# Kernel optimization log

Measured on AMD Instinct MI355X. Metric: run time of the kernel, lower is better.

The kernel has to match this reference:

```python
import jax, jax.numpy as jnp
import numpy as np

B, D = 8, 256
MEM, CW, R, K, KL = 131072, 64, 4, 4, 4
C = R * K + 2 * KL + 1  # 25 visible cells
DELTA = 0.005
EPS = 1e-6
TIMESTEP = 1.0  # first step after reset


def _gather(x, idx):
    # x: (b,m) or (b,m,w); idx: (b,k)
    if x.ndim == 2:
        return jnp.take_along_axis(x, idx, axis=1)
    e = jnp.broadcast_to(idx[:, :, None], idx.shape + (x.shape[-1],))
    return jnp.take_along_axis(x, e, axis=1)


def _fwd(xi, memory, visible_memory, link_matrix, rev_link_matrix, precedence,
         read_weights, write_weights, usage,
         W_rq, b_rq, W_wv, b_wv, W_ig, b_ig, W_wg, b_wg,
         read_positions):
    b = xi.shape[0]
    bidx = jnp.arange(b)[:, None]

    # interface transforms (independent linears)
    read_query = (xi @ W_rq + b_rq).reshape(b, R, CW)      # (b,r,w)
    write_vector = (xi @ W_wv + b_wv).reshape(b, 1, CW)    # (b,1,w)
    ig = jax.nn.sigmoid(xi @ W_ig + b_ig)                  # (b,c)
    wg = jax.nn.sigmoid(xi @ W_wg + b_wg)                  # (b,1)

    # ------------------ write ------------------
    rw_vis = _gather(read_weights, read_positions)         # (b,c)
    ww_vis = _gather(write_weights, read_positions)        # (b,c)

    # usage update + least-used indicator over visible cells
    u = (rw_vis + ww_vis > DELTA).astype(memory.dtype)
    rel = _gather(usage, read_positions)
    I_min = (rel == jnp.min(rel, axis=-1, keepdims=True)).astype(memory.dtype)
    rel_new = (TIMESTEP - rel) * u + rel * (1.0 - u)
    usage = usage.at[bidx, read_positions].set(rel_new)

    # interpolated write weights over visible cells
    ww_new = wg * (ig * rw_vis + (1.0 - ig) * I_min)       # (b,c)
    write_weights = write_weights.at[bidx, read_positions].set(ww_new)

    # erase + write into visible memory, scatter back into sparse memory
    visible_memory = visible_memory * (1.0 - I_min[:, :, None]) + ww_new[:, :, None] * write_vector
    memory = memory.at[bidx, read_positions].set(visible_memory)

    # link matrix / reverse link matrix update
    trp = read_positions[:, R * K:R * K + 2 * KL]          # temporal positions (b,2KL)
    Ieye = jnp.eye(MEM, 2 * KL, dtype=memory.dtype)[None]  # eye(m,k) mask as in torch code
    prec_dense = jnp.zeros_like(write_weights).at[bidx, trp].set(precedence)  # (b,m)
    tww = _gather(write_weights, trp)                      # (b,2KL)
    link_matrix = ((1.0 - write_weights[:, :, None]) * link_matrix
                   + write_weights[:, :, None] * precedence[:, None, :]) * Ieye
    rev_link_matrix = ((1.0 - tww[:, None, :]) * rev_link_matrix
                       + tww[:, None, :] * prec_dense[:, :, None]) * Ieye

    # precedence update and least-used cell (argmin usage)
    precedence = (1.0 - jnp.sum(tww, axis=-1, keepdims=True)) * precedence + tww
    least_used = jax.lax.top_k(-usage, 1)[1]               # (b,1)

    # ------------------ read ------------------
    trw = _gather(read_weights, trp)                       # (b,2KL)
    fwd_w = jnp.einsum('bmk,bk->bm', link_matrix, trw)     # forward weighting
    bwd_w = jnp.einsum('bmk,bk->bm', rev_link_matrix, trw) # backward weighting

    # exact L2 k-NN over full memory (dense surrogate for the FAISS search)
    mem_sq = jnp.sum(memory * memory, axis=-1)             # (b,m)
    dots = jnp.einsum('brw,bmw->brm', read_query, memory)  # (b,r,m)
    knn = jax.lax.top_k(2.0 * dots - mem_sq[:, None, :], K)[1].reshape(b, R * K)

    fp = jax.lax.top_k(fwd_w, KL)[1]
    bp = jax.lax.top_k(bwd_w, KL)[1]
    lum = jnp.full((b, 1), C + 1, dtype=knn.dtype)         # timestep <= mem_size branch
    max_length = least_used[0, 0]                          # mem_limit_reached == False
    positions = jnp.clip(
        jnp.concatenate([knn, fp.astype(knn.dtype), bp.astype(knn.dtype), lum], axis=1),
        0, max_length)                                     # (b,c)

    visible = _gather(memory, positions)                   # (b,c,w)
    kq = read_query / (jnp.linalg.norm(read_query, axis=-1, keepdims=True) + EPS)
    vn = visible / (jnp.linalg.norm(visible, axis=-1, keepdims=True) + EPS)
    sim = jnp.einsum('brw,bcw->brc', kq, vn)               # cosine similarity
    rw_c = jax.nn.softmax(sim, axis=-1)                    # (b,r,c)
    read_vectors = jnp.einsum('brc,bcw->brw', rw_c, visible)
    return read_vectors


def setup_inputs() -> dict:
    key = jax.random.key(0)
    ks = jax.random.split(key, 16)
    inp = {}
    inp['xi'] = jax.random.normal(ks[0], (B, D), jnp.float32)
    inp['memory'] = jax.random.normal(ks[1], (B, MEM, CW), jnp.float32)
    inp['visible_memory'] = jax.random.normal(ks[2], (B, C, CW), jnp.float32)
    inp['link_matrix'] = 0.1 * jax.random.uniform(ks[3], (B, MEM, 2 * KL), jnp.float32)
    inp['rev_link_matrix'] = 0.1 * jax.random.uniform(ks[4], (B, MEM, 2 * KL), jnp.float32)
    inp['precedence'] = 0.1 * jax.random.uniform(ks[5], (B, 2 * KL), jnp.float32)
    inp['read_weights'] = 0.01 * jax.random.uniform(ks[6], (B, MEM), jnp.float32)
    inp['write_weights'] = 0.01 * jax.random.uniform(ks[7], (B, MEM), jnp.float32)
    usage = 0.5 + 0.5 * jax.random.uniform(ks[8], (B, MEM), jnp.float32)
    inp['usage'] = usage.at[:, MEM - 1].set(0.0)  # argmin lands at m-1 so the clamp is a no-op
    inp['least_used_mem'] = jnp.full((B, 1), MEM // 2, jnp.int32)
    inp['read_positions'] = jax.random.randint(ks[9], (B, C), 0, MEM)

    def lin(k, fi, fo):
        s = (6.0 / fi) ** 0.5  # kaiming-uniform-like
        return jax.random.uniform(k, (fi, fo), jnp.float32, -s, s)
    inp['W_rq'] = lin(ks[10], D, R * CW); inp['b_rq'] = jnp.zeros((R * CW,), jnp.float32)
    inp['W_wv'] = lin(ks[11], D, CW);     inp['b_wv'] = jnp.zeros((CW,), jnp.float32)
    inp['W_ig'] = lin(ks[12], D, C);      inp['b_ig'] = jnp.zeros((C,), jnp.float32)
    inp['W_wg'] = lin(ks[13], D, 1);      inp['b_wg'] = jnp.zeros((1,), jnp.float32)
    return inp


def reference(xi, memory, visible_memory, link_matrix, rev_link_matrix, precedence,
              read_weights, write_weights, usage, least_used_mem, read_positions,
              W_rq, b_rq, W_wv, b_wv, W_ig, b_ig, W_wg, b_wg):
    # least_used_mem is overwritten inside write() (argmin of updated usage) before use
    return _fwd(xi, memory, visible_memory, link_matrix, rev_link_matrix, precedence,
                read_weights, write_weights, usage,
                W_rq, b_rq, W_wv, b_wv, W_ig, b_ig, W_wg, b_wg,
                read_positions)
```

## Files before the change

### kernel.cpp

```cpp
#include <hip/hip_runtime.h>
#include <math.h>

#define BN 8
#define DDIM 256
#define MEMN 131072
#define CWN 64
#define RN 4
#define CN 25
#define DELTA_C 0.005f
#define EPS_C 1e-6f
#define RPB 1024
#define NBLK (MEMN / RPB)
#define NEG_INF (-3.402823466e38f)
#define IMAX 0x7fffffff
#define UPD_STRIDE 32


__device__ inline void wave_reduce_max(float& v, int& i, int& t) {
#pragma unroll
  for (int off = 32; off; off >>= 1) {
    float ov = __shfl_down(v, off);
    int oi = __shfl_down(i, off);
    int ot = __shfl_down(t, off);
    if (ov > v || (ov == v && oi < i)) { v = ov; i = oi; t = ot; }
  }
}

__device__ inline void block_argmax256(int tid, float v, int i, int t,
                                       float& rv, int& ri, int& rt) {
  __shared__ float sv[4];
  __shared__ int si[4], st[4];
  __shared__ float bv;
  __shared__ int bi, bt;
  wave_reduce_max(v, i, t);
  if ((tid & 63) == 0) { int w = tid >> 6; sv[w] = v; si[w] = i; st[w] = t; }
  __syncthreads();
  if (tid == 0) {
    float xv = sv[0]; int xi = si[0], xt = st[0];
#pragma unroll
    for (int w = 1; w < 4; w++)
      if (sv[w] > xv || (sv[w] == xv && si[w] < xi)) { xv = sv[w]; xi = si[w]; xt = st[w]; }
    bv = xv; bi = xi; bt = xt;
  }
  __syncthreads();
  rv = bv; ri = bi; rt = bt;
  __syncthreads();
}

__device__ inline void top4_of8(const float* v8, int* out4) {
  float val[12]; int idx[12]; bool used[12];
#pragma unroll
  for (int i = 0; i < 12; i++) { val[i] = (i < 8) ? v8[i] : 0.f; idx[i] = i; used[i] = false; }
  for (int r = 0; r < 4; r++) {
    int best = -1;
    for (int i = 0; i < 12; i++) {
      if (used[i]) continue;
      if (best < 0 || val[i] > val[best]) best = i;
    }
    used[best] = true;
    out4[r] = idx[best];
  }
}

__global__ __launch_bounds__(256) void k12_heads_state(
    const float* __restrict__ xi,
    const float* __restrict__ Wrq, const float* __restrict__ brq,
    const float* __restrict__ Wwv, const float* __restrict__ bwv,
    const float* __restrict__ Wig, const float* __restrict__ big,
    const float* __restrict__ Wwg, const float* __restrict__ bwg,
    const float* __restrict__ vm, const float* __restrict__ prec,
    const float* __restrict__ rw, const float* __restrict__ wwg,
    const float* __restrict__ usage,
    const float* __restrict__ lm, const float* __restrict__ rlm,
    const int* __restrict__ rp,
    float* rq, int* fp, int* bp,
    int* upd_pos, float* upd_rel, float* upd_mem) {
  int b = blockIdx.x, tid = threadIdx.x;
  __shared__ float x[DDIM];
  __shared__ float wv_s[64], ig_s[CN], wg_s;
  __shared__ int pos[CN];
  __shared__ float s_rw[CN], s_ww[CN], s_rel[CN], s_relnew[CN], s_imin[CN], s_wwnew[CN];
  __shared__ int s_guard[CN];
  __shared__ float minrel;
  __shared__ float fwd8[8], bwd8[8];

  x[tid] = xi[b * DDIM + tid];
  __syncthreads();
  {
    float s = brq[tid];
#pragma unroll 8
    for (int d = 0; d < DDIM; d++) s = fmaf(x[d], Wrq[d * 256 + tid], s);
    rq[b * 256 + tid] = s;
  }
  if (tid < 64) {
    float s = bwv[tid];
#pragma unroll 8
    for (int d = 0; d < DDIM; d++) s = fmaf(x[d], Wwv[d * 64 + tid], s);
    wv_s[tid] = s;
  } else if (tid < 64 + CN) {
    int o = tid - 64;
    float s = big[o];
#pragma unroll 8
    for (int d = 0; d < DDIM; d++) s = fmaf(x[d], Wig[d * CN + o], s);
    ig_s[o] = 1.f / (1.f + expf(-s));
  } else if (tid == 64 + CN) {
    float s = bwg[0];
#pragma unroll 8
    for (int d = 0; d < DDIM; d++) s = fmaf(x[d], Wwg[d], s);
    wg_s = 1.f / (1.f + expf(-s));
  }
  if (tid < CN) {
    int p = rp[b * CN + tid];
    pos[tid] = p;
    s_rw[tid] = rw[(size_t)b * MEMN + p];
    s_ww[tid] = wwg[(size_t)b * MEMN + p];
    s_rel[tid] = usage[(size_t)b * MEMN + p];
  }
  __syncthreads();
  if (tid == 0) {
    float m = s_rel[0];
    for (int j = 1; j < CN; j++) m = fminf(m, s_rel[j]);
    minrel = m;
  }
  __syncthreads();
  if (tid < CN) {
    float u = (s_rw[tid] + s_ww[tid] > DELTA_C) ? 1.f : 0.f;
    float im = (s_rel[tid] == minrel) ? 1.f : 0.f;
    s_imin[tid] = im;
    s_relnew[tid] = u * (1.f - s_rel[tid]) + (1.f - u) * s_rel[tid];
    float igv = ig_s[tid];
    s_wwnew[tid] = wg_s * (igv * s_rw[tid] + (1.f - igv) * im);
    int g = 1;
    for (int j = tid + 1; j < CN; j++)
      if (pos[j] == pos[tid]) { g = 0; break; }
    s_guard[tid] = g;
  }
  __syncthreads();
  if (tid < CN) {
    upd_pos[b * UPD_STRIDE + tid] = s_guard[tid] ? pos[tid] : -1;
    upd_rel[b * UPD_STRIDE + tid] = s_relnew[tid];
  }
  for (int it = 0; it < 7; it++) {
    int j = it * 4 + (tid >> 6);
    int lane = tid & 63;
    if (j < CN && s_guard[j]) {
      float v = vm[((size_t)b * CN + j) * 64 + lane] * (1.f - s_imin[j]) +
                s_wwnew[j] * wv_s[lane];
      upd_mem[((size_t)b * CN + j) * 64 + lane] = v;
    }
  }
  __syncthreads();
  if (tid < 8) {
    int m = tid;
    int trp_m = pos[16 + m];
    float tww = 0.f;
    for (int j = CN - 1; j >= 0; j--)
      if (pos[j] == trp_m) { tww = s_wwnew[j]; break; }
    float trw = rw[(size_t)b * MEMN + trp_m];
    float wwu;
    {
      int found = -1;
      for (int j = CN - 1; j >= 0; j--)
        if (pos[j] == m) { found = j; break; }
      wwu = (found >= 0) ? s_wwnew[found] : wwg[(size_t)b * MEMN + m];
    }
    float lmd = (1.f - wwu) * lm[((size_t)b * MEMN + m) * 8 + m] + wwu * prec[b * 8 + m];
    float pd = 0.f;
    for (int k = 7; k >= 0; k--)
      if (pos[16 + k] == m) { pd = prec[b * 8 + k]; break; }
    float rld = (1.f - tww) * rlm[((size_t)b * MEMN + m) * 8 + m] + tww * pd;
    fwd8[m] = lmd * trw;
    bwd8[m] = rld * trw;
  }
  __syncthreads();
  if (tid == 0) top4_of8(fwd8, &fp[b * 4]);
  if (tid == 1) top4_of8(bwd8, &bp[b * 4]);
}

__global__ __launch_bounds__(256) void k3_scan(
    const float* __restrict__ memory, const float* __restrict__ usage,
    const float* __restrict__ rq,
    const int* __restrict__ upd_pos, const float* __restrict__ upd_rel,
    const float* __restrict__ upd_mem,
    float* blk_sv, int* blk_si, float* blk_uv, int* blk_ui) {
  int tid = threadIdx.x;
  int b = blockIdx.x / NBLK;
  int blk = blockIdx.x % NBLK;
  int base = blk * RPB;
  int wave = tid >> 6, lane = tid & 63;
  int sub = lane & 15;
  int grp = lane >> 4;

  __shared__ int s_lcnt;
  __shared__ int s_lpos[CN], s_lj[CN];
  __shared__ float s_lrel[CN];
  if (tid == 0) s_lcnt = 0;
  __syncthreads();
  if (tid < CN) {
    int p = upd_pos[b * UPD_STRIDE + tid];
    if (p >= base && p < base + RPB) {
      int k = atomicAdd(&s_lcnt, 1);
      s_lpos[k] = p;
      s_lj[k] = tid;
      s_lrel[k] = upd_rel[b * UPD_STRIDE + tid];
    }
  }
  __syncthreads();
  int lcnt = s_lcnt;
  const float4* upd4 = (const float4*)upd_mem;

  const float4* q4 = (const float4*)(rq + b * 256);
  float4 qf0 = q4[0 * 16 + sub];
  float4 qf1 = q4[1 * 16 + sub];
  float4 qf2 = q4[2 * 16 + sub];
  float4 qf3 = q4[3 * 16 + sub];

  float tv0 = NEG_INF, tv1 = NEG_INF, tv2 = NEG_INF, tv3 = NEG_INF;
  int ti0 = IMAX, ti1 = IMAX, ti2 = IMAX, ti3 = IMAX;

  int rowbase = base + wave * 256;
  const float4* mp = (const float4*)memory;
  size_t lanebase = ((size_t)b * MEMN + rowbase) * 16 + (size_t)grp * 16 + sub;

#pragma unroll 4
  for (int it = 0; it < 64; it++) {
    int m = rowbase + it * 4 + grp;
    float4 x = mp[lanebase + (size_t)it * 64];
    if (lcnt) {
      for (int k = 0; k < lcnt; k++)
        if (m == s_lpos[k])
          x = upd4[((size_t)b * CN + s_lj[k]) * 16 + sub];
    }
    float d0 = fmaf(x.x, qf0.x, fmaf(x.y, qf0.y, fmaf(x.z, qf0.z, x.w * qf0.w)));
    float d1 = fmaf(x.x, qf1.x, fmaf(x.y, qf1.y, fmaf(x.z, qf1.z, x.w * qf1.w)));
    float d2 = fmaf(x.x, qf2.x, fmaf(x.y, qf2.y, fmaf(x.z, qf2.z, x.w * qf2.w)));
    float d3 = fmaf(x.x, qf3.x, fmaf(x.y, qf3.y, fmaf(x.z, qf3.z, x.w * qf3.w)));
    float sq = fmaf(x.x, x.x, fmaf(x.y, x.y, fmaf(x.z, x.z, x.w * x.w)));
#pragma unroll
    for (int off = 1; off < 16; off <<= 1) {
      d0 += __shfl_xor(d0, off);
      d1 += __shfl_xor(d1, off);
      d2 += __shfl_xor(d2, off);
      d3 += __shfl_xor(d3, off);
      sq += __shfl_xor(sq, off);
    }
    float d = (sub == 0) ? d0 : (sub == 1) ? d1 : (sub == 2) ? d2 : d3;
    float s = 2.f * d - sq;
    if (sub < 4) {
      if (s > tv3) {
        tv3 = s; ti3 = m;
        if (tv3 > tv2) { float t = tv2; tv2 = tv3; tv3 = t; int u = ti2; ti2 = ti3; ti3 = u; }
        if (tv2 > tv1) { float t = tv1; tv1 = tv2; tv2 = t; int u = ti1; ti1 = ti2; ti2 = u; }
        if (tv1 > tv0) { float t = tv0; tv0 = tv1; tv1 = t; int u = ti0; ti0 = ti1; ti1 = u; }
      }
    }
  }

  __shared__ float lsv[4][16][4];
  __shared__ int lsi[4][16][4];
  if (sub < 4) {
    int slot = wave * 4 + grp;
    lsv[sub][slot][0] = tv0; lsi[sub][slot][0] = ti0;
    lsv[sub][slot][1] = tv1; lsi[sub][slot][1] = ti1;
    lsv[sub][slot][2] = tv2; lsi[sub][slot][2] = ti2;
    lsv[sub][slot][3] = tv3; lsi[sub][slot][3] = ti3;
  }
  __syncthreads();
  {
    int w = wave;
    float v = lsv[w][lane >> 2][lane & 3];
    int i = lsi[w][lane >> 2][lane & 3];
    size_t o = (((size_t)b * 4 + w) * NBLK + blk) * 4;
    for (int round = 0; round < 4; round++) {
      float rv = v; int ri = i; int rt = lane;
      wave_reduce_max(rv, ri, rt);
      rv = __shfl(rv, 0); ri = __shfl(ri, 0); rt = __shfl(rt, 0);
      if (lane == 0) { blk_sv[o + round] = rv; blk_si[o + round] = ri; }
      if (lane == rt) { v = NEG_INF; i = IMAX; }
    }
  }

  if (b == 0) {
    const float4* u4 = (const float4*)(usage + base);
    float4 uu = u4[tid];
    int mb = base + tid * 4;
    if (lcnt) {
      for (int k = 0; k < lcnt; k++) {
        int d = s_lpos[k] - mb;
        if ((unsigned)d < 4u) {
          float rv = s_lrel[k];
          if (d == 0) uu.x = rv;
          else if (d == 1) uu.y = rv;
          else if (d == 2) uu.z = rv;
          else uu.w = rv;
        }
      }
    }
    float uv = uu.x; int uix = mb;
    if (uu.y < uv) { uv = uu.y; uix = mb + 1; }
    if (uu.z < uv) { uv = uu.z; uix = mb + 2; }
    if (uu.w < uv) { uv = uu.w; uix = mb + 3; }
    float rvv; int rii, rtt;
    block_argmax256(tid, -uv, uix, tid, rvv, rii, rtt);
    if (tid == 0) {
      blk_uv[blk] = -rvv;
      blk_ui[blk] = rii;
    }
  }
}

__global__ __launch_bounds__(256) void k45_merge_attn(
    const float* __restrict__ memory, const float* __restrict__ rq,
    const float* __restrict__ blk_sv, const int* __restrict__ blk_si,
    const float* __restrict__ blk_uv, const int* __restrict__ blk_ui,
    const int* __restrict__ fp, const int* __restrict__ bp,
    const int* __restrict__ upd_pos, const float* __restrict__ upd_mem,
    float* out) {
  int b = blockIdx.x, tid = threadIdx.x;
  int wave = tid >> 6, lane = tid & 63;
  __shared__ int knn_s[16];
  __shared__ int sL;
  __shared__ int pos[CN];
  __shared__ int supd[CN];
  __shared__ int ovr[CN];
  __shared__ float vis[CN][64];
  __shared__ float vnorm[CN];
  __shared__ float rnorm[4];
  __shared__ float sim[4][CN];
  __shared__ float pw[4][CN];
  __shared__ float qs[4][64];

  {
    int r = wave;
    size_t o = (size_t)(b * 4 + r) * NBLK * 4;
    float tv0 = NEG_INF, tv1 = NEG_INF, tv2 = NEG_INF, tv3 = NEG_INF;
    int ti0 = IMAX, ti1 = IMAX, ti2 = IMAX, ti3 = IMAX;
#pragma unroll
    for (int j = 0; j < 8; j++) {
      float s = blk_sv[o + j * 64 + lane];
      int m = blk_si[o + j * 64 + lane];
      if (s > tv3) {
        tv3 = s; ti3 = m;
        if (tv3 > tv2) { float t = tv2; tv2 = tv3; tv3 = t; int u = ti2; ti2 = ti3; ti3 = u; }
        if (tv2 > tv1) { float t = tv1; tv1 = tv2; tv2 = t; int u = ti1; ti1 = ti2; ti2 = u; }
        if (tv1 > tv0) { float t = tv0; tv0 = tv1; tv1 = t; int u = ti0; ti0 = ti1; ti1 = u; }
      }
    }
    for (int round = 0; round < 4; round++) {
      float rv = tv0; int ri = ti0; int rt = lane;
      wave_reduce_max(rv, ri, rt);
      rv = __shfl(rv, 0); ri = __shfl(ri, 0); rt = __shfl(rt, 0);
      if (lane == 0) knn_s[r * 4 + round] = ri;
      if (lane == rt) {
        tv0 = tv1; ti0 = ti1; tv1 = tv2; ti1 = ti2;
        tv2 = tv3; ti2 = ti3; tv3 = NEG_INF; ti3 = IMAX;
      }
    }
  }
  if (wave == 0) {
    float u0 = blk_uv[lane], u1 = blk_uv[64 + lane];
    int i0 = blk_ui[lane], i1 = blk_ui[64 + lane];
    float v; int i;
    if (u1 < u0 || (u1 == u0 && i1 < i0)) { v = u1; i = i1; } else { v = u0; i = i0; }
    float rv = -v; int ri = i; int rt = lane;
    wave_reduce_max(rv, ri, rt);
    if (lane == 0) sL = ri;
  }
  qs[tid >> 6][tid & 63] = rq[b * 256 + tid];
  __syncthreads();

  int L = sL;
  if (tid < CN) {
    supd[tid] = upd_pos[b * UPD_STRIDE + tid];
    int v;
    if (tid < 16) v = knn_s[tid];
    else if (tid < 20) v = fp[b * 4 + tid - 16];
    else if (tid < 24) v = bp[b * 4 + tid - 20];
    else v = CN + 1;
    v = min(v, L);
    v = max(v, 0);
    pos[tid] = v;
  }
  __syncthreads();
  if (tid < CN) {
    int o = -1;
    for (int j = 0; j < CN; j++)
      if (supd[j] == pos[tid]) o = j;
    ovr[tid] = o;
  }
  __syncthreads();
  for (int it = 0; it < 7; it++) {
    int j = it * 4 + (tid >> 6);
    int ln = tid & 63;
    if (j < CN) {
      int o = ovr[j];
      vis[j][ln] = (o >= 0)
          ? upd_mem[((size_t)b * CN + o) * 64 + ln]
          : memory[((size_t)b * MEMN + pos[j]) * 64 + ln];
    }
  }
  __syncthreads();
  if (tid < CN) {
    float s = 0.f;
    for (int k = 0; k < 64; k++) s = fmaf(vis[tid][k], vis[tid][k], s);
    vnorm[tid] = sqrtf(s) + EPS_C;
  }
  if (tid >= 32 && tid < 36) {
    int r = tid - 32;
    float s = 0.f;
    for (int k = 0; k < 64; k++) s = fmaf(qs[r][k], qs[r][k], s);
    rnorm[r] = sqrtf(s) + EPS_C;
  }
  __syncthreads();
  if (tid < 4 * CN) {
    int r = tid / CN, c = tid % CN;
    float s = 0.f;
    for (int k = 0; k < 64; k++) s = fmaf(qs[r][k], vis[c][k], s);
    sim[r][c] = s / (rnorm[r] * vnorm[c]);
  }
  __syncthreads();
  if (tid < 4) {
    int r = tid;
    float mx = NEG_INF;
    for (int c = 0; c < CN; c++) mx = fmaxf(mx, sim[r][c]);
    float sum = 0.f;
    for (int c = 0; c < CN; c++) { float e = expf(sim[r][c] - mx); pw[r][c] = e; sum += e; }
    float inv = 1.f / sum;
    for (int c = 0; c < CN; c++) pw[r][c] *= inv;
  }
  __syncthreads();
  {
    int r = tid >> 6, w = tid & 63;
    float s = 0.f;
    for (int c = 0; c < CN; c++) s = fmaf(pw[r][c], vis[c][w], s);
    out[(size_t)b * 256 + tid] = s;
  }
}

extern "C" void kernel_launch(void* const* d_in, const int* in_sizes, int n_in,
                              void* d_out, int out_size, void* d_ws, size_t ws_size,
                              hipStream_t stream) {
  const float* xi = (const float*)d_in[0];
  const float* memory = (const float*)d_in[1];
  const float* vm = (const float*)d_in[2];
  const float* lm = (const float*)d_in[3];
  const float* rlm = (const float*)d_in[4];
  const float* prec = (const float*)d_in[5];
  const float* rw = (const float*)d_in[6];
  const float* wwg = (const float*)d_in[7];
  const float* usage = (const float*)d_in[8];
  const int* rp = (const int*)d_in[10];
  const float* Wrq = (const float*)d_in[11];
  const float* brq = (const float*)d_in[12];
  const float* Wwv = (const float*)d_in[13];
  const float* bwv = (const float*)d_in[14];
  const float* Wig = (const float*)d_in[15];
  const float* big = (const float*)d_in[16];
  const float* Wwg = (const float*)d_in[17];
  const float* bwg = (const float*)d_in[18];
  float* out = (float*)d_out;

  float* f = (float*)d_ws;
  float* rq_w = f;      f += BN * 256;
  float* upd_mem_w = f; f += (size_t)BN * CN * 64;
  float* upd_rel_w = f; f += BN * UPD_STRIDE;
  float* blk_sv = f;    f += (size_t)BN * 4 * NBLK * 4;
  float* blk_uv = f;    f += NBLK;
  int* ip = (int*)f;
  int* upd_pos_w = ip;  ip += BN * UPD_STRIDE;
  int* fp_w = ip;       ip += BN * 4;
  int* bp_w = ip;       ip += BN * 4;
  int* blk_si = ip;     ip += (size_t)BN * 4 * NBLK * 4;
  int* blk_ui = ip;     ip += NBLK;

  hipLaunchKernelGGL(k12_heads_state, dim3(BN), dim3(256), 0, stream,
                     xi, Wrq, brq, Wwv, bwv, Wig, big, Wwg, bwg,
                     vm, prec, rw, wwg, usage, lm, rlm, rp,
                     rq_w, fp_w, bp_w, upd_pos_w, upd_rel_w, upd_mem_w);
  hipLaunchKernelGGL(k3_scan, dim3(BN * NBLK), dim3(256), 0, stream,
                     memory, usage, rq_w, upd_pos_w, upd_rel_w, upd_mem_w,
                     blk_sv, blk_si, blk_uv, blk_ui);
  hipLaunchKernelGGL(k45_merge_attn, dim3(BN), dim3(256), 0, stream,
                     memory, rq_w, blk_sv, blk_si, blk_uv, blk_ui,
                     fp_w, bp_w, upd_pos_w, upd_mem_w, out);
}
```

Measured before the change: 495.0 us.

## Fuse three kernels into one mega-kernel with last-block merge

Merges the head/state kernel, the memory scan, and the merge/attention kernel into a single launch. Every scan block recomputes the interface linears and write state locally in shared memory, so the intermediate global buffers go away. The least-used reduction now goes through a 64-bit atomicMax key, and the last block per batch, found with an atomic counter, performs the final merge and attention. This removes two kernel launches and their global round trips. In exchange, each of the 1024 blocks redoes the 256x256 matvec, and the last blocks for b>0 spin-wait on counters[0], which risks deadlock or contention.

```diff
diff --git a/kernel.cpp b/kernel.cpp
--- a/kernel.cpp
+++ b/kernel.cpp
@@ -13,7 +13,6 @@
 #define NBLK (MEMN / RPB)
 #define NEG_INF (-3.402823466e38f)
 #define IMAX 0x7fffffff
-#define UPD_STRIDE 32
 
 
 __device__ inline void wave_reduce_max(float& v, int& i, int& t) {
@@ -62,7 +61,7 @@
   }
 }
 
-__global__ __launch_bounds__(256) void k12_heads_state(
+__global__ __launch_bounds__(256, 4) void mega(
     const float* __restrict__ xi,
     const float* __restrict__ Wrq, const float* __restrict__ brq,
     const float* __restrict__ Wwv, const float* __restrict__ bwv,
@@ -73,24 +72,47 @@
     const float* __restrict__ usage,
     const float* __restrict__ lm, const float* __restrict__ rlm,
     const int* __restrict__ rp,
-    float* rq, int* fp, int* bp,
-    int* upd_pos, float* upd_rel, float* upd_mem) {
-  int b = blockIdx.x, tid = threadIdx.x;
+    const float* __restrict__ memory,
+    float* blk_sv, int* blk_si,
+    unsigned int* counters, unsigned long long* ukey,
+    float* out) {
+  int tid = threadIdx.x;
+  int b = blockIdx.x / NBLK;
+  int blk = blockIdx.x % NBLK;
+  int base = blk * RPB;
+  int wave = tid >> 6, lane = tid & 63;
+  int sub = lane & 15;
+  int grp = lane >> 4;
+
   __shared__ float x[DDIM];
+  __shared__ __align__(16) float rq_s[DDIM];
   __shared__ float wv_s[64], ig_s[CN], wg_s;
-  __shared__ int pos[CN];
+  __shared__ int ppos[CN];
   __shared__ float s_rw[CN], s_ww[CN], s_rel[CN], s_relnew[CN], s_imin[CN], s_wwnew[CN];
   __shared__ int s_guard[CN];
   __shared__ float minrel;
   __shared__ float fwd8[8], bwd8[8];
+  __shared__ int fp_s[4], bp_s[4];
+  __shared__ __align__(16) float upd_lds[CN][64];
+  __shared__ int s_lcnt;
+  __shared__ int s_lpos[CN], s_lj[CN];
+  __shared__ float s_lrel[CN];
+  __shared__ float lsv[4][16][4];
+  __shared__ int lsi[4][16][4];
+  __shared__ int is_last;
+  __shared__ int knn_s[16];
+  __shared__ float vis[CN][64];
+  __shared__ float vnorm[CN], rnorm[4];
+  __shared__ float sim[4][CN], pw[4][CN];
 
   x[tid] = xi[b * DDIM + tid];
+  if (tid == 0) s_lcnt = 0;
   __syncthreads();
   {
     float s = brq[tid];
 #pragma unroll 8
     for (int d = 0; d < DDIM; d++) s = fmaf(x[d], Wrq[d * 256 + tid], s);
-    rq[b * 256 + tid] = s;
+    rq_s[tid] = s;
   }
   if (tid < 64) {
     float s = bwv[tid];
@@ -111,7 +133,7 @@
   }
   if (tid < CN) {
     int p = rp[b * CN + tid];
-    pos[tid] = p;
+    ppos[tid] = p;
     s_rw[tid] = rw[(size_t)b * MEMN + p];
     s_ww[tid] = wwg[(size_t)b * MEMN + p];
     s_rel[tid] = usage[(size_t)b * MEMN + p];
@@ -132,84 +154,55 @@
     s_wwnew[tid] = wg_s * (igv * s_rw[tid] + (1.f - igv) * im);
     int g = 1;
     for (int j = tid + 1; j < CN; j++)
-      if (pos[j] == pos[tid]) { g = 0; break; }
+      if (ppos[j] == ppos[tid]) { g = 0; break; }
     s_guard[tid] = g;
   }
   __syncthreads();
-  if (tid < CN) {
-    upd_pos[b * UPD_STRIDE + tid] = s_guard[tid] ? pos[tid] : -1;
-    upd_rel[b * UPD_STRIDE + tid] = s_relnew[tid];
-  }
   for (int it = 0; it < 7; it++) {
-    int j = it * 4 + (tid >> 6);
-    int lane = tid & 63;
+    int j = it * 4 + wave;
     if (j < CN && s_guard[j]) {
-      float v = vm[((size_t)b * CN + j) * 64 + lane] * (1.f - s_imin[j]) +
-                s_wwnew[j] * wv_s[lane];
-      upd_mem[((size_t)b * CN + j) * 64 + lane] = v;
-    }
-  }
-  __syncthreads();
+      upd_lds[j][lane] = vm[((size_t)b * CN + j) * 64 + lane] * (1.f - s_imin[j]) +
+                         s_wwnew[j] * wv_s[lane];
+    }
+  }
   if (tid < 8) {
     int m = tid;
-    int trp_m = pos[16 + m];
+    int trp_m = ppos[16 + m];
     float tww = 0.f;
     for (int j = CN - 1; j >= 0; j--)
-      if (pos[j] == trp_m) { tww = s_wwnew[j]; break; }
+      if (ppos[j] == trp_m) { tww = s_wwnew[j]; break; }
     float trw = rw[(size_t)b * MEMN + trp_m];
     float wwu;
     {
       int found = -1;
       for (int j = CN - 1; j >= 0; j--)
-        if (pos[j] == m) { found = j; break; }
+        if (ppos[j] == m) { found = j; break; }
       wwu = (found >= 0) ? s_wwnew[found] : wwg[(size_t)b * MEMN + m];
     }
     float lmd = (1.f - wwu) * lm[((size_t)b * MEMN + m) * 8 + m] + wwu * prec[b * 8 + m];
     float pd = 0.f;
     for (int k = 7; k >= 0; k--)
-      if (pos[16 + k] == m) { pd = prec[b * 8 + k]; break; }
+      if (ppos[16 + k] == m) { pd = prec[b * 8 + k]; break; }
     float rld = (1.f - tww) * rlm[((size_t)b * MEMN + m) * 8 + m] + tww * pd;
     fwd8[m] = lmd * trw;
     bwd8[m] = rld * trw;
   }
   __syncthreads();
-  if (tid == 0) top4_of8(fwd8, &fp[b * 4]);
-  if (tid == 1) top4_of8(bwd8, &bp[b * 4]);
-}
-
-__global__ __launch_bounds__(256) void k3_scan(
-    const float* __restrict__ memory, const float* __restrict__ usage,
-    const float* __restrict__ rq,
-    const int* __restrict__ upd_pos, const float* __restrict__ upd_rel,
-    const float* __restrict__ upd_mem,
-    float* blk_sv, int* blk_si, float* blk_uv, int* blk_ui) {
-  int tid = threadIdx.x;
-  int b = blockIdx.x / NBLK;
-  int blk = blockIdx.x % NBLK;
-  int base = blk * RPB;
-  int wave = tid >> 6, lane = tid & 63;
-  int sub = lane & 15;
-  int grp = lane >> 4;
-
-  __shared__ int s_lcnt;
-  __shared__ int s_lpos[CN], s_lj[CN];
-  __shared__ float s_lrel[CN];
-  if (tid == 0) s_lcnt = 0;
-  __syncthreads();
-  if (tid < CN) {
-    int p = upd_pos[b * UPD_STRIDE + tid];
+  if (tid == 0) top4_of8(fwd8, fp_s);
+  if (tid == 1) top4_of8(bwd8, bp_s);
+  if (tid < CN) {
+    int p = s_guard[tid] ? ppos[tid] : -1;
     if (p >= base && p < base + RPB) {
       int k = atomicAdd(&s_lcnt, 1);
       s_lpos[k] = p;
       s_lj[k] = tid;
-      s_lrel[k] = upd_rel[b * UPD_STRIDE + tid];
-    }
-  }
-  __syncthreads();
+      s_lrel[k] = s_relnew[tid];
+    }
+  }
+  __syncthreads();
+
   int lcnt = s_lcnt;
-  const float4* upd4 = (const float4*)upd_mem;
-
-  const float4* q4 = (const float4*)(rq + b * 256);
+  const float4* q4 = (const float4*)rq_s;
   float4 qf0 = q4[0 * 16 + sub];
   float4 qf1 = q4[1 * 16 + sub];
   float4 qf2 = q4[2 * 16 + sub];
@@ -225,17 +218,17 @@
 #pragma unroll 4
   for (int it = 0; it < 64; it++) {
     int m = rowbase + it * 4 + grp;
-    float4 x = mp[lanebase + (size_t)it * 64];
+    float4 xx = mp[lanebase + (size_t)it * 64];
     if (lcnt) {
       for (int k = 0; k < lcnt; k++)
         if (m == s_lpos[k])
-          x = upd4[((size_t)b * CN + s_lj[k]) * 16 + sub];
-    }
-    float d0 = fmaf(x.x, qf0.x, fmaf(x.y, qf0.y, fmaf(x.z, qf0.z, x.w * qf0.w)));
-    float d1 = fmaf(x.x, qf1.x, fmaf(x.y, qf1.y, fmaf(x.z, qf1.z, x.w * qf1.w)));
-    float d2 = fmaf(x.x, qf2.x, fmaf(x.y, qf2.y, fmaf(x.z, qf2.z, x.w * qf2.w)));
-    float d3 = fmaf(x.x, qf3.x, fmaf(x.y, qf3.y, fmaf(x.z, qf3.z, x.w * qf3.w)));
-    float sq = fmaf(x.x, x.x, fmaf(x.y, x.y, fmaf(x.z, x.z, x.w * x.w)));
+          xx = ((const float4*)upd_lds[s_lj[k]])[sub];
+    }
+    float d0 = fmaf(xx.x, qf0.x, fmaf(xx.y, qf0.y, fmaf(xx.z, qf0.z, xx.w * qf0.w)));
+    float d1 = fmaf(xx.x, qf1.x, fmaf(xx.y, qf1.y, fmaf(xx.z, qf1.z, xx.w * qf1.w)));
+    float d2 = fmaf(xx.x, qf2.x, fmaf(xx.y, qf2.y, fmaf(xx.z, qf2.z, xx.w * qf2.w)));
+    float d3 = fmaf(xx.x, qf3.x, fmaf(xx.y, qf3.y, fmaf(xx.z, qf3.z, xx.w * qf3.w)));
+    float sq = fmaf(xx.x, xx.x, fmaf(xx.y, xx.y, fmaf(xx.z, xx.z, xx.w * xx.w)));
 #pragma unroll
     for (int off = 1; off < 16; off <<= 1) {
       d0 += __shfl_xor(d0, off);
@@ -256,8 +249,6 @@
     }
   }
 
-  __shared__ float lsv[4][16][4];
-  __shared__ int lsi[4][16][4];
   if (sub < 4) {
     int slot = wave * 4 + grp;
     lsv[sub][slot][0] = tv0; lsi[sub][slot][0] = ti0;
@@ -303,100 +294,85 @@
     float rvv; int rii, rtt;
     block_argmax256(tid, -uv, uix, tid, rvv, rii, rtt);
     if (tid == 0) {
-      blk_uv[blk] = -rvv;
-      blk_ui[blk] = rii;
-    }
-  }
-}
-
-__global__ __launch_bounds__(256) void k45_merge_attn(
-    const float* __restrict__ memory, const float* __restrict__ rq,
-    const float* __restrict__ blk_sv, const int* __restrict__ blk_si,
-    const float* __restrict__ blk_uv, const int* __restrict__ blk_ui,
-    const int* __restrict__ fp, const int* __restrict__ bp,
-    const int* __restrict__ upd_pos, const float* __restrict__ upd_mem,
-    float* out) {
-  int b = blockIdx.x, tid = threadIdx.x;
-  int wave = tid >> 6, lane = tid & 63;
-  __shared__ int knn_s[16];
-  __shared__ int sL;
-  __shared__ int pos[CN];
-  __shared__ int supd[CN];
-  __shared__ int ovr[CN];
-  __shared__ float vis[CN][64];
-  __shared__ float vnorm[CN];
-  __shared__ float rnorm[4];
-  __shared__ float sim[4][CN];
-  __shared__ float pw[4][CN];
-  __shared__ float qs[4][64];
+      unsigned vb = __float_as_uint(-rvv);
+      unsigned long long key =
+          ((unsigned long long)(0xFFFFFFFFu - vb) << 32) | (0xFFFFFFFFu - (unsigned)rii);
+      atomicMax(ukey, key);
+    }
+  }
+
+  __syncthreads();
+  __threadfence();
+  if (tid == 0) is_last = (atomicAdd(&counters[b], 1u) == (unsigned)(NBLK - 1));
+  __syncthreads();
+  if (!is_last) return;
+  if (tid == 0 && b != 0) {
+    while (atomicAdd(&counters[0], 0u) < (unsigned)NBLK) {}
+  }
+  __syncthreads();
+  __threadfence();
 
   {
     int r = wave;
     size_t o = (size_t)(b * 4 + r) * NBLK * 4;
-    float tv0 = NEG_INF, tv1 = NEG_INF, tv2 = NEG_INF, tv3 = NEG_INF;
-    int ti0 = IMAX, ti1 = IMAX, ti2 = IMAX, ti3 = IMAX;
+    float av0 = NEG_INF, av1 = NEG_INF, av2 = NEG_INF, av3 = NEG_INF;
+    int ai0 = IMAX, ai1 = IMAX, ai2 = IMAX, ai3 = IMAX;
 #pragma unroll
     for (int j = 0; j < 8; j++) {
       float s = blk_sv[o + j * 64 + lane];
       int m = blk_si[o + j * 64 + lane];
-      if (s > tv3) {
-        tv3 = s; ti3 = m;
-        if (tv3 > tv2) { float t = tv2; tv2 = tv3; tv3 = t; int u = ti2; ti2 = ti3; ti3 = u; }
-        if (tv2 > tv1) { float t = tv1; tv1 = tv2; tv2 = t; int u = ti1; ti1 = ti2; ti2 = u; }
-        if (tv1 > tv0) { float t = tv0; tv0 = tv1; tv1 = t; int u = ti0; ti0 = ti1; ti1 = u; }
+      if (s > av3) {
+        av3 = s; ai3 = m;
+        if (av3 > av2) { float t = av2; av2 = av3; av3 = t; int u = ai2; ai2 = ai3; ai3 = u; }
+        if (av2 > av1) { float t = av1; av1 = av2; av2 = t; int u = ai1; ai1 = ai2; ai2 = u; }
+        if (av1 > av0) { float t = av0; av0 = av1; av1 = t; int u = ai0; ai0 = ai1; ai1 = u; }
       }
     }
     for (int round = 0; round < 4; round++) {
-      float rv = tv0; int ri = ti0; int rt = lane;
+      float rv = av0; int ri = ai0; int rt = lane;
       wave_reduce_max(rv, ri, rt);
       rv = __shfl(rv, 0); ri = __shfl(ri, 0); rt = __shfl(rt, 0);
       if (lane == 0) knn_s[r * 4 + round] = ri;
       if (lane == rt) {
-        tv0 = tv1; ti0 = ti1; tv1 = tv2; ti1 = ti2;
-        tv2 = tv3; ti2 = ti3; tv3 = NEG_INF; ti3 = IMAX;
+        av0 = av1; ai0 = ai1; av1 = av2; ai1 = ai2;
+        av2 = av3; ai2 = ai3; av3 = NEG_INF; ai3 = IMAX;
       }
     }
   }
-  if (wave == 0) {
-    float u0 = blk_uv[lane], u1 = blk_uv[64 + lane];
-    int i0 = blk_ui[lane], i1 = blk_ui[64 + lane];
-    float v; int i;
-    if (u1 < u0 || (u1 == u0 && i1 < i0)) { v = u1; i = i1; } else { v = u0; i = i0; }
-    float rv = -v; int ri = i; int rt = lane;
-    wave_reduce_max(rv, ri, rt);
-    if (lane == 0) sL = ri;
-  }
-  qs[tid >> 6][tid & 63] = rq[b * 256 + tid];
-  __syncthreads();
-
-  int L = sL;
-  if (tid < CN) {
-    supd[tid] = upd_pos[b * UPD_STRIDE + tid];
+  __syncthreads();
+
+  int L;
+  {
+    unsigned long long k = *(volatile unsigned long long*)ukey;
+    L = (int)(0xFFFFFFFFu - (unsigned)(k & 0xFFFFFFFFull));
+  }
+  __shared__ int cpos[CN];
+  __shared__ int ovr[CN];
+  if (tid < CN) {
     int v;
     if (tid < 16) v = knn_s[tid];
-    else if (tid < 20) v = fp[b * 4 + tid - 16];
-    else if (tid < 24) v = bp[b * 4 + tid - 20];
+    else if (tid < 20) v = fp_s[tid - 16];
+    else if (tid < 24) v = bp_s[tid - 20];
     else v = CN + 1;
     v = min(v, L);
     v = max(v, 0);
-    pos[tid] = v;
+    cpos[tid] = v;
   }
   __syncthreads();
   if (tid < CN) {
     int o = -1;
     for (int j = 0; j < CN; j++)
-      if (supd[j] == pos[tid]) o = j;
+      if (s_guard[j] && ppos[j] == cpos[tid]) o = j;
     ovr[tid] = o;
   }
   __syncthreads();
   for (int it = 0; it < 7; it++) {
-    int j = it * 4 + (tid >> 6);
-    int ln = tid & 63;
+    int j = it * 4 + wave;
     if (j < CN) {
       int o = ovr[j];
-      vis[j][ln] = (o >= 0)
-          ? upd_mem[((size_t)b * CN + o) * 64 + ln]
-          : memory[((size_t)b * MEMN + pos[j]) * 64 + ln];
+      vis[j][lane] = (o >= 0)
+          ? upd_lds[o][lane]
+          : memory[((size_t)b * MEMN + cpos[j]) * 64 + lane];
     }
   }
   __syncthreads();
@@ -408,14 +384,14 @@
   if (tid >= 32 && tid < 36) {
     int r = tid - 32;
     float s = 0.f;
-    for (int k = 0; k < 64; k++) s = fmaf(qs[r][k], qs[r][k], s);
+    for (int k = 0; k < 64; k++) s = fmaf(rq_s[r * 64 + k], rq_s[r * 64 + k], s);
     rnorm[r] = sqrtf(s) + EPS_C;
   }
   __syncthreads();
   if (tid < 4 * CN) {
     int r = tid / CN, c = tid % CN;
     float s = 0.f;
-    for (int k = 0; k < 64; k++) s = fmaf(qs[r][k], vis[c][k], s);
+    for (int k = 0; k < 64; k++) s = fmaf(rq_s[r * 64 + k], vis[c][k], s);
     sim[r][c] = s / (rnorm[r] * vnorm[c]);
   }
   __syncthreads();
@@ -430,7 +406,7 @@
   }
   __syncthreads();
   {
-    int r = tid >> 6, w = tid & 63;
+    int r = wave, w = lane;
     float s = 0.f;
     for (int c = 0; c < CN; c++) s = fmaf(pw[r][c], vis[c][w], s);
     out[(size_t)b * 256 + tid] = s;
@@ -460,27 +436,14 @@
   const float* bwg = (const float*)d_in[18];
   float* out = (float*)d_out;
 
-  float* f = (float*)d_ws;
-  float* rq_w = f;      f += BN * 256;
-  float* upd_mem_w = f; f += (size_t)BN * CN * 64;
-  float* upd_rel_w = f; f += BN * UPD_STRIDE;
-  float* blk_sv = f;    f += (size_t)BN * 4 * NBLK * 4;
-  float* blk_uv = f;    f += NBLK;
-  int* ip = (int*)f;
-  int* upd_pos_w = ip;  ip += BN * UPD_STRIDE;
-  int* fp_w = ip;       ip += BN * 4;
-  int* bp_w = ip;       ip += BN * 4;
-  int* blk_si = ip;     ip += (size_t)BN * 4 * NBLK * 4;
-  int* blk_ui = ip;     ip += NBLK;
-
-  hipLaunchKernelGGL(k12_heads_state, dim3(BN), dim3(256), 0, stream,
+  unsigned int* counters = (unsigned int*)d_ws;
+  unsigned long long* ukey = (unsigned long long*)((char*)d_ws + 32);
+  float* blk_sv = (float*)((char*)d_ws + 64);
+  int* blk_si = (int*)(blk_sv + (size_t)BN * 4 * NBLK * 4);
+
+  hipMemsetAsync(d_ws, 0, 64, stream);
+  hipLaunchKernelGGL(mega, dim3(BN * NBLK), dim3(256), 0, stream,
                      xi, Wrq, brq, Wwv, bwv, Wig, big, Wwg, bwg,
-                     vm, prec, rw, wwg, usage, lm, rlm, rp,
-                     rq_w, fp_w, bp_w, upd_pos_w, upd_rel_w, upd_mem_w);
-  hipLaunchKernelGGL(k3_scan, dim3(BN * NBLK), dim3(256), 0, stream,
-                     memory, usage, rq_w, upd_pos_w, upd_rel_w, upd_mem_w,
-                     blk_sv, blk_si, blk_uv, blk_ui);
-  hipLaunchKernelGGL(k45_merge_attn, dim3(BN), dim3(256), 0, stream,
-                     memory, rq_w, blk_sv, blk_si, blk_uv, blk_ui,
-                     fp_w, bp_w, upd_pos_w, upd_mem_w, out);
+                     vm, prec, rw, wwg, usage, lm, rlm, rp, memory,
+                     blk_sv, blk_si, counters, ukey, out);
 }
```

New measurement: 620.6 us. +25.4%, slower.

## Remap scan so four lanes share each memory row, cutting shuffle reductions

Applied to the files above, without the earlier changes.

The memory scan kernel now assigns each memory row to four lanes that each load 16 floats (four float4s), instead of sixteen lanes loading one float4 each. The cross-lane reduction for the four query dot products and the squared norm shrinks from four shuffle steps to two, and every lane keeps its own top-4 list, so the lanes that previously sat idle in selection now do useful work. The block-level merge is rewritten so each lane holds a sorted list of four and pops its head when it wins a round. Costs are more registers for the query fragments (a launch bound of 4 blocks per SM is added), more shared memory for the partial lists, and strided 64-byte per-lane loads rather than fully contiguous wave loads.

```diff
diff --git a/kernel.cpp b/kernel.cpp
--- a/kernel.cpp
+++ b/kernel.cpp
@@ -60,6 +60,10 @@
     used[best] = true;
     out4[r] = idx[best];
   }
+}
+
+__device__ inline float dot4(float4 a, float4 b) {
+  return fmaf(a.x, b.x, fmaf(a.y, b.y, fmaf(a.z, b.z, a.w * b.w)));
 }
 
 __global__ __launch_bounds__(256) void k12_heads_state(
@@ -177,7 +181,7 @@
   if (tid == 1) top4_of8(bwd8, &bp[b * 4]);
 }
 
-__global__ __launch_bounds__(256) void k3_scan(
+__global__ __launch_bounds__(256, 4) void k3_scan(
     const float* __restrict__ memory, const float* __restrict__ usage,
     const float* __restrict__ rq,
     const int* __restrict__ upd_pos, const float* __restrict__ upd_rel,
@@ -188,8 +192,7 @@
   int blk = blockIdx.x % NBLK;
   int base = blk * RPB;
   int wave = tid >> 6, lane = tid & 63;
-  int sub = lane & 15;
-  int grp = lane >> 4;
+  int r4 = lane >> 2, s4 = lane & 3;
 
   __shared__ int s_lcnt;
   __shared__ int s_lpos[CN], s_lj[CN];
@@ -210,73 +213,88 @@
   const float4* upd4 = (const float4*)upd_mem;
 
   const float4* q4 = (const float4*)(rq + b * 256);
-  float4 qf0 = q4[0 * 16 + sub];
-  float4 qf1 = q4[1 * 16 + sub];
-  float4 qf2 = q4[2 * 16 + sub];
-  float4 qf3 = q4[3 * 16 + sub];
+  float4 qf[4][4];
+#pragma unroll
+  for (int q = 0; q < 4; q++)
+#pragma unroll
+    for (int j = 0; j < 4; j++)
+      qf[q][j] = q4[q * 16 + s4 * 4 + j];
 
   float tv0 = NEG_INF, tv1 = NEG_INF, tv2 = NEG_INF, tv3 = NEG_INF;
   int ti0 = IMAX, ti1 = IMAX, ti2 = IMAX, ti3 = IMAX;
 
-  int rowbase = base + wave * 256;
+  int rowstart = base + wave * 256;
   const float4* mp = (const float4*)memory;
-  size_t lanebase = ((size_t)b * MEMN + rowbase) * 16 + (size_t)grp * 16 + sub;
-
-#pragma unroll 4
-  for (int it = 0; it < 64; it++) {
-    int m = rowbase + it * 4 + grp;
-    float4 x = mp[lanebase + (size_t)it * 64];
+
+#pragma unroll 2
+  for (int bi = 0; bi < 16; bi++) {
+    int m = rowstart + bi * 16 + r4;
+    size_t a = ((size_t)b * MEMN + m) * 16 + s4 * 4;
+    float4 x0 = mp[a + 0];
+    float4 x1 = mp[a + 1];
+    float4 x2 = mp[a + 2];
+    float4 x3 = mp[a + 3];
     if (lcnt) {
       for (int k = 0; k < lcnt; k++)
-        if (m == s_lpos[k])
-          x = upd4[((size_t)b * CN + s_lj[k]) * 16 + sub];
-    }
-    float d0 = fmaf(x.x, qf0.x, fmaf(x.y, qf0.y, fmaf(x.z, qf0.z, x.w * qf0.w)));
-    float d1 = fmaf(x.x, qf1.x, fmaf(x.y, qf1.y, fmaf(x.z, qf1.z, x.w * qf1.w)));
-    float d2 = fmaf(x.x, qf2.x, fmaf(x.y, qf2.y, fmaf(x.z, qf2.z, x.w * qf2.w)));
-    float d3 = fmaf(x.x, qf3.x, fmaf(x.y, qf3.y, fmaf(x.z, qf3.z, x.w * qf3.w)));
-    float sq = fmaf(x.x, x.x, fmaf(x.y, x.y, fmaf(x.z, x.z, x.w * x.w)));
-#pragma unroll
-    for (int off = 1; off < 16; off <<= 1) {
+        if (m == s_lpos[k]) {
+          const float4* u = &upd4[((size_t)b * CN + s_lj[k]) * 16 + s4 * 4];
+          x0 = u[0]; x1 = u[1]; x2 = u[2]; x3 = u[3];
+        }
+    }
+    float d0 = (dot4(x0, qf[0][0]) + dot4(x1, qf[0][1])) +
+               (dot4(x2, qf[0][2]) + dot4(x3, qf[0][3]));
+    float d1 = (dot4(x0, qf[1][0]) + dot4(x1, qf[1][1])) +
+               (dot4(x2, qf[1][2]) + dot4(x3, qf[1][3]));
+    float d2 = (dot4(x0, qf[2][0]) + dot4(x1, qf[2][1])) +
+               (dot4(x2, qf[2][2]) + dot4(x3, qf[2][3]));
+    float d3 = (dot4(x0, qf[3][0]) + dot4(x1, qf[3][1])) +
+               (dot4(x2, qf[3][2]) + dot4(x3, qf[3][3]));
+    float sq = (dot4(x0, x0) + dot4(x1, x1)) +
+               (dot4(x2, x2) + dot4(x3, x3));
+#pragma unroll
+    for (int off = 1; off < 4; off <<= 1) {
       d0 += __shfl_xor(d0, off);
       d1 += __shfl_xor(d1, off);
       d2 += __shfl_xor(d2, off);
       d3 += __shfl_xor(d3, off);
       sq += __shfl_xor(sq, off);
     }
-    float d = (sub == 0) ? d0 : (sub == 1) ? d1 : (sub == 2) ? d2 : d3;
+    float d = (s4 == 0) ? d0 : (s4 == 1) ? d1 : (s4 == 2) ? d2 : d3;
     float s = 2.f * d - sq;
-    if (sub < 4) {
-      if (s > tv3) {
-        tv3 = s; ti3 = m;
-        if (tv3 > tv2) { float t = tv2; tv2 = tv3; tv3 = t; int u = ti2; ti2 = ti3; ti3 = u; }
-        if (tv2 > tv1) { float t = tv1; tv1 = tv2; tv2 = t; int u = ti1; ti1 = ti2; ti2 = u; }
-        if (tv1 > tv0) { float t = tv0; tv0 = tv1; tv1 = t; int u = ti0; ti0 = ti1; ti1 = u; }
-      }
-    }
-  }
-
-  __shared__ float lsv[4][16][4];
-  __shared__ int lsi[4][16][4];
-  if (sub < 4) {
-    int slot = wave * 4 + grp;
-    lsv[sub][slot][0] = tv0; lsi[sub][slot][0] = ti0;
-    lsv[sub][slot][1] = tv1; lsi[sub][slot][1] = ti1;
-    lsv[sub][slot][2] = tv2; lsi[sub][slot][2] = ti2;
-    lsv[sub][slot][3] = tv3; lsi[sub][slot][3] = ti3;
+    if (s > tv3) {
+      tv3 = s; ti3 = m;
+      if (tv3 > tv2) { float t = tv2; tv2 = tv3; tv3 = t; int u = ti2; ti2 = ti3; ti3 = u; }
+      if (tv2 > tv1) { float t = tv1; tv1 = tv2; tv2 = t; int u = ti1; ti1 = ti2; ti2 = u; }
+      if (tv1 > tv0) { float t = tv0; tv0 = tv1; tv1 = t; int u = ti0; ti0 = ti1; ti1 = u; }
+    }
+  }
+
+  __shared__ float lsv[4][64][4];
+  __shared__ int lsi[4][64][4];
+  {
+    int slot = wave * 16 + r4;
+    lsv[s4][slot][0] = tv0; lsi[s4][slot][0] = ti0;
+    lsv[s4][slot][1] = tv1; lsi[s4][slot][1] = ti1;
+    lsv[s4][slot][2] = tv2; lsi[s4][slot][2] = ti2;
+    lsv[s4][slot][3] = tv3; lsi[s4][slot][3] = ti3;
   }
   __syncthreads();
   {
     int w = wave;
-    float v = lsv[w][lane >> 2][lane & 3];
-    int i = lsi[w][lane >> 2][lane & 3];
+    float v0 = lsv[w][lane][0], v1 = lsv[w][lane][1],
+          v2 = lsv[w][lane][2], v3 = lsv[w][lane][3];
+    int i0 = lsi[w][lane][0], i1 = lsi[w][lane][1],
+        i2 = lsi[w][lane][2], i3 = lsi[w][lane][3];
     size_t o = (((size_t)b * 4 + w) * NBLK + blk) * 4;
     for (int round = 0; round < 4; round++) {
-      float rv = v; int ri = i; int rt = lane;
+      float rv = v0; int ri = i0; int rt = lane;
       wave_reduce_max(rv, ri, rt);
       rv = __shfl(rv, 0); ri = __shfl(ri, 0); rt = __shfl(rt, 0);
       if (lane == 0) { blk_sv[o + round] = rv; blk_si[o + round] = ri; }
-      if (lane == rt) { v = NEG_INF; i = IMAX; }
+      if (lane == rt) {
+        v0 = v1; i0 = i1; v1 = v2; i1 = i2;
+        v2 = v3; i2 = i3; v3 = NEG_INF; i3 = IMAX;
+      }
     }
   }
 
```

Measured after the change: 489.4 us. About the same (-1.1%).
